# Performance work log

Measured on AMD Instinct MI355X. Metric: run time of the kernel, lower is better.

## Reference

```python
import jax, jax.numpy as jnp
import numpy as np

# Static architecture constants (match init_kwargs)
N, M, DIM = 2048, 4096, 256
KS = (0.9, 0.8, 0.7)
HEADS, BOT_HEADS = 4, 2
NEG_SLOPE = 0.2  # PyG GATConv default leaky-relu slope


def _p(key, shape, scale):
    return (scale * jax.random.normal(key, shape, dtype=jnp.float32))


def setup_inputs() -> dict:
    key = jax.random.key(0)
    ks = jax.random.split(key, 16)
    # Symmetric positive connectivity matrix (fMRI-like), fully dense
    R = jax.random.uniform(ks[0], (N, N), dtype=jnp.float32)
    A = 0.5 * (R + R.T)
    X = jax.random.normal(ks[1], (N, DIM), dtype=jnp.float32)
    s = 1.0 / np.sqrt(DIM).astype(np.float32)
    C, Cb = DIM // HEADS, DIM // BOT_HEADS
    inp = {
        'A': A, 'X': X,
        'W_down': _p(ks[2], (3, DIM, DIM), s),
        'as_down': _p(ks[3], (3, HEADS, C), s),
        'ad_down': _p(ks[4], (3, HEADS, C), s),
        'b_down': jnp.zeros((3, DIM), jnp.float32),
        'W_up': _p(ks[5], (3, DIM, DIM), s),
        'as_up': _p(ks[6], (3, HEADS, C), s),
        'ad_up': _p(ks[7], (3, HEADS, C), s),
        'b_up': jnp.zeros((3, DIM), jnp.float32),
        'W_bot': _p(ks[8], (DIM, DIM), s),
        'as_bot': _p(ks[9], (BOT_HEADS, Cb), s),
        'ad_bot': _p(ks[10], (BOT_HEADS, Cb), s),
        'b_bot': jnp.zeros((DIM,), jnp.float32),
        'W_pool': _p(ks[11], (3, DIM), s),
        'b_pool': jnp.zeros((3,), jnp.float32),
        'W_ups': _p(ks[12], (M, N), 1.0 / np.sqrt(N).astype(np.float32)),
        'b_ups': jnp.zeros((M,), jnp.float32),
    }
    return inp


def _sym_norm(A):
    # A_tilde = A + I ; D^{-1/2} A_tilde D^{-1/2} as elementwise broadcast
    A = A + jnp.eye(A.shape[0], dtype=A.dtype)
    d = A.sum(axis=1) + 1e-5
    di = d ** -0.5
    return di[:, None] * A * di[None, :]


def _gat(A, X, W, a_src, a_dst, b):
    # Dense-masked GATConv (concat=True, eval mode => no dropout).
    # Edge j->i exists iff A[j, i] > 0 (dense_to_sparse row=src, col=tgt).
    n = X.shape[0]
    H, C = a_src.shape
    x = (X @ W).reshape(n, H, C)                       # [n, H, C]
    s = jnp.einsum('nhc,hc->nh', x, a_src)             # source logit term
    t = jnp.einsum('nhc,hc->nh', x, a_dst)             # target logit term
    logits = jax.nn.leaky_relu(t[:, None, :] + s[None, :, :], NEG_SLOPE)  # [i, j, h]
    mask = (A.T > 0)[:, :, None]
    attn = jax.nn.softmax(jnp.where(mask, logits, -jnp.inf), axis=1)
    out = jnp.einsum('ijh,jhc->ihc', attn, x).reshape(n, H * C) + b
    return jax.nn.relu(out)


def reference(A, X, W_down, as_down, ad_down, b_down,
              W_up, as_up, ad_up, b_up,
              W_bot, as_bot, ad_bot, b_bot,
              W_pool, b_pool, W_ups, b_ups):
    A = _sym_norm(A)
    A_hist, idx_hist = [], []
    # Encoder: GAT -> top-k pool (gather rows/cols)
    for i in range(3):
        X = _gat(A, X, W_down[i], as_down[i], ad_down[i], b_down[i])
        A_hist.append(A)
        scores = jax.nn.sigmoid(X @ W_pool[i] + b_pool[i])
        k = max(2, int(KS[i] * A.shape[0]))            # static sizes
        vals, idx = jax.lax.top_k(scores, k)
        X = X[idx] * vals[:, None]
        A = A[idx][:, idx]
        idx_hist.append(idx)
    X = _gat(A, X, W_bot, as_bot, ad_bot, b_bot)
    # Decoder: scatter-unpool -> GAT -> adjacency reconstruction
    for i in range(3):
        u = 2 - i
        A, idx = A_hist[u], idx_hist[u]
        Xn = jnp.zeros((A.shape[0], X.shape[1]), X.dtype).at[idx].set(X)
        X = _gat(A, Xn, W_up[i], as_up[i], ad_up[i], b_up[i])
    # Upsampler: Linear(n->m) on X^T, then A_up = relu(Xu Xu^T)
    X_up = W_ups @ X + b_ups[:, None]                  # [M, DIM]
    A_up = jax.nn.relu(X_up @ X_up.T)                  # [M, M]
    return A_up
```

## Files before the change

### kernel.cpp

```cpp
#include <hip/hip_runtime.h>
#include <math.h>

#define NEG 0.2f
#define NMAX 2048
#define CHUNK 64
#define NCHMAX 32

__device__ __forceinline__ float lrelu(float v) { return v > 0.f ? v : NEG * v; }
__device__ __forceinline__ unsigned fenc(float v) {
    unsigned u = __float_as_uint(v);
    return (u & 0x80000000u) ? ~u : (u | 0x80000000u);
}
__device__ __forceinline__ float fdec(unsigned u) {
    return (u & 0x80000000u) ? __uint_as_float(u ^ 0x80000000u) : __uint_as_float(~u);
}

__global__ __launch_bounds__(256) void gemm_ks(const float* __restrict__ A,
                                               const float* __restrict__ B,
                                               float* __restrict__ C,
                                               const int* __restrict__ rowmapA,
                                               const float* __restrict__ rowscale,
                                               const int* __restrict__ rowmapC,
                                               int M, int N, int K) {
    __shared__ float As[16][68];
    __shared__ float Bs[16][68];
    const int tid = threadIdx.x;
    const int m0 = blockIdx.x * 64, n0 = blockIdx.y * 64;
    const int kchunk = K / gridDim.z;
    const int kbeg = blockIdx.z * kchunk, kend = kbeg + kchunk;
    const int tm = tid >> 4, tn = tid & 15;
    const int lr = tid >> 2, lc4 = (tid & 3) * 4;
    const int br = tid >> 4, bc4 = (tid & 15) * 4;
    const int am = m0 + lr;
    const bool aval = am < M;
    int arow = 0; float ascale = 1.f;
    if (aval) { arow = rowmapA ? rowmapA[am] : am; if (rowscale) ascale = rowscale[arow]; }
    const float* Ap = A + (size_t)arow * K;
    float4 va = make_float4(0.f, 0.f, 0.f, 0.f), vb;
    if (aval) va = *(const float4*)(Ap + kbeg + lc4);
    vb = *(const float4*)(B + (size_t)(kbeg + br) * N + n0 + bc4);
    float acc[4][4] = {{0.f}};
    for (int k0 = kbeg; k0 < kend; k0 += 16) {
        As[lc4 + 0][lr] = va.x * ascale; As[lc4 + 1][lr] = va.y * ascale;
        As[lc4 + 2][lr] = va.z * ascale; As[lc4 + 3][lr] = va.w * ascale;
        *(float4*)&Bs[br][bc4] = vb;
        __syncthreads();
        if (k0 + 16 < kend) {
            if (aval) va = *(const float4*)(Ap + k0 + 16 + lc4);
            vb = *(const float4*)(B + (size_t)(k0 + 16 + br) * N + n0 + bc4);
        }
#pragma unroll
        for (int kk = 0; kk < 16; ++kk) {
            float a[4], b[4];
            *(float4*)a = *(const float4*)&As[kk][tm * 4];
            *(float4*)b = *(const float4*)&Bs[kk][tn * 4];
#pragma unroll
            for (int x = 0; x < 4; ++x)
#pragma unroll
                for (int y = 0; y < 4; ++y) acc[x][y] = fmaf(a[x], b[y], acc[x][y]);
        }
        __syncthreads();
    }
#pragma unroll
    for (int x = 0; x < 4; ++x) {
        int m = m0 + tm * 4 + x;
        if (m >= M) continue;
        int orow = rowmapC ? rowmapC[m] : m;
        float* dst = C + (size_t)orow * N + n0 + tn * 4;
#pragma unroll
        for (int y = 0; y < 4; ++y) atomicAdd(dst + y, acc[x][y]);
    }
}

__global__ __launch_bounds__(256) void st_kernel(const float* __restrict__ xw,
                                                 const float* __restrict__ asrc,
                                                 const float* __restrict__ adst,
                                                 float* __restrict__ S, float* __restrict__ T,
                                                 unsigned* __restrict__ SMX,
                                                 int n, int Hh, int Cc) {
    int gid = blockIdx.x * 256 + threadIdx.x;
    int i = gid / Hh, h = gid - i * Hh;
    float s = -INFINITY;
    if (i < n) {
        const float* xr = xw + (size_t)i * 256 + h * Cc;
        const float* pa = asrc + h * Cc;
        const float* pd = adst + h * Cc;
        float sv = 0.f, tv = 0.f;
        for (int c = 0; c < Cc; c += 4) {
            float4 xv = *(const float4*)(xr + c);
            float4 av = *(const float4*)(pa + c);
            float4 dv = *(const float4*)(pd + c);
            sv += xv.x * av.x + xv.y * av.y + xv.z * av.z + xv.w * av.w;
            tv += xv.x * dv.x + xv.y * dv.y + xv.z * dv.z + xv.w * dv.w;
        }
        S[(size_t)i * Hh + h] = sv;
        T[(size_t)i * Hh + h] = tv;
        s = sv;
    }
    for (int off = Hh; off < 64; off <<= 1) s = fmaxf(s, __shfl_xor(s, off));
    int lane = threadIdx.x & 63;
    if (lane < Hh && s > -INFINITY) atomicMax(SMX + lane, fenc(s));
}

__global__ __launch_bounds__(256) void rank_k(const float* __restrict__ S,
                                              float* __restrict__ SS, int* __restrict__ PERM,
                                              int n, int Hh) {
    __shared__ float s[NMAX];
    int h = blockIdx.y;
    for (int j = threadIdx.x; j < n; j += 256) s[j] = S[(size_t)j * Hh + h];
    __syncthreads();
    int i = blockIdx.x * 256 + threadIdx.x;
    if (i >= n) return;
    float v = s[i];
    int cnt = 0, j = 0;
    for (; j + 4 <= n; j += 4) {
        float4 sv = *(const float4*)&s[j];
        cnt += (sv.x > v) || (sv.x == v && (j + 0) < i);
        cnt += (sv.y > v) || (sv.y == v && (j + 1) < i);
        cnt += (sv.z > v) || (sv.z == v && (j + 2) < i);
        cnt += (sv.w > v) || (sv.w == v && (j + 3) < i);
    }
    for (; j < n; ++j) {
        float sj = s[j];
        cnt += (sj > v) || (sj == v && j < i);
    }
    SS[h * NMAX + cnt] = v;
    PERM[h * NMAX + cnt] = i;
}

__global__ __launch_bounds__(256) void chunk_k(const float* __restrict__ XW,
                                               const float* __restrict__ SS,
                                               const int* __restrict__ PERM,
                                               const unsigned* __restrict__ SMX,
                                               float* __restrict__ TOT1, float* __restrict__ TOT2,
                                               float* __restrict__ ZT1, float* __restrict__ ZT2,
                                               int n, int Cc) {
    const int h = blockIdx.x, ch = blockIdx.y;
    const int nh = 256 / Cc, seg = CHUNK / nh;
    const int c = threadIdx.x % Cc, half = threadIdx.x / Cc;
    __shared__ float ssh[CHUNK];
    __shared__ int pjh[CHUNK];
    __shared__ float red1[256], red2[256];
    __shared__ float zr1[4], zr2[4];
    if (threadIdx.x < CHUNK) {
        int rk = ch * CHUNK + threadIdx.x;
        ssh[threadIdx.x] = (rk < n) ? SS[h * NMAX + rk] : 0.f;
        pjh[threadIdx.x] = (rk < n) ? PERM[h * NMAX + rk] : -1;
    }
    __syncthreads();
    const float smax = fdec(SMX[h]);
    float t1 = 0.f, t2 = 0.f, z1 = 0.f, z2 = 0.f;
#pragma unroll 4
    for (int q = 0; q < seg; ++q) {
        int r = half * seg + q;
        int j = pjh[r];
        if (j < 0) continue;
        float d = ssh[r] - smax;
        float w1 = expf(d), w2 = expf(NEG * d);
        float x = XW[(size_t)j * 256 + h * Cc + c];
        t1 = fmaf(w1, x, t1); t2 = fmaf(w2, x, t2);
        z1 += w1; z2 += w2;
    }
    red1[threadIdx.x] = t1; red2[threadIdx.x] = t2;
    if (c == 0) { zr1[half] = z1; zr2[half] = z2; }
    __syncthreads();
    if (half == 0) {
        for (int hh = 1; hh < nh; ++hh) { t1 += red1[hh * Cc + c]; t2 += red2[hh * Cc + c]; }
        TOT1[((size_t)h * NCHMAX + ch) * Cc + c] = t1;
        TOT2[((size_t)h * NCHMAX + ch) * Cc + c] = t2;
        if (c == 0) {
            float a = z1, b = z2;
            for (int hh = 1; hh < nh; ++hh) { a += zr1[hh]; b += zr2[hh]; }
            ZT1[h * NCHMAX + ch] = a;
            ZT2[h * NCHMAX + ch] = b;
        }
    }
}

__global__ __launch_bounds__(256) void combine_k(
    const float* __restrict__ XW, const float* __restrict__ SS,
    const int* __restrict__ PERM, const unsigned* __restrict__ SMX,
    const float* __restrict__ T,
    const float* __restrict__ TOT1, const float* __restrict__ TOT2,
    const float* __restrict__ ZT1, const float* __restrict__ ZT2,
    const float* __restrict__ bias, const float* __restrict__ Wp,
    const float* __restrict__ bp,
    float* __restrict__ Xout, float* __restrict__ SC, int n, int Hh, int nch) {
    const int i = blockIdx.x, t = threadIdx.x;
    const int C = 256 / Hh;
    __shared__ float f1s[4], f2s[4], invs[4], smaxs[4];
    __shared__ int qs[4], chs[4];
    __shared__ float coef[256];
    __shared__ int permsh[256];
    __shared__ float redw[4];
    float z1p = 0.f, z2s = 0.f;
    if (t < Hh) {
        int h = t;
        float smax = fdec(SMX[h]);
        smaxs[h] = smax;
        float tv = T[(size_t)i * Hh + h];
        float u = tv + smax, m = lrelu(u);
        f1s[h] = expf(u - m);
        f2s[h] = expf(NEG * u - m);
        float thr = -tv;
        int lo = 0, hi = n;
        while (lo < hi) {
            int mid = (lo + hi) >> 1;
            if (SS[h * NMAX + mid] > thr) lo = mid + 1; else hi = mid;
        }
        int q = lo;
        int ch = min(q / CHUNK, nch - 1);
        qs[h] = q; chs[h] = ch;
        for (int cc = 0; cc < ch; ++cc) z1p += ZT1[h * NCHMAX + cc];
        for (int cc = ch + 1; cc < nch; ++cc) z2s += ZT2[h * NCHMAX + cc];
    }
    __syncthreads();
    if (t < Hh * CHUNK) {
        int h = t >> 6, r = t & 63;
        int rank = chs[h] * CHUNK + r;
        float w = 0.f; int j = 0;
        if (rank < n) {
            float ssv = SS[h * NMAX + rank];
            j = PERM[h * NMAX + rank];
            float d = ssv - smaxs[h];
            w = (rank < qs[h]) ? f1s[h] * expf(d) : f2s[h] * expf(NEG * d);
        }
        coef[t] = w; permsh[t] = j;
    }
    __syncthreads();
    if (t < Hh) {
        int h = t;
        float den = fmaf(f1s[h], z1p, f2s[h] * z2s);
        for (int r = 0; r < CHUNK; ++r) den += coef[h * CHUNK + r];
        invs[h] = 1.f / den;
    }
    __syncthreads();
    const int h = t / C, c = t - h * C;
    const float* xcol = XW + h * C + c;
    float csum = 0.f;
#pragma unroll 8
    for (int r = 0; r < CHUNK; ++r)
        csum = fmaf(coef[h * CHUNK + r], xcol[(size_t)permsh[h * CHUNK + r] * 256], csum);
    float a1 = 0.f, a2 = 0.f;
    const int ch = chs[h];
    for (int cc = 0; cc < ch; ++cc) a1 += TOT1[((size_t)h * NCHMAX + cc) * C + c];
    for (int cc = ch + 1; cc < nch; ++cc) a2 += TOT2[((size_t)h * NCHMAX + cc) * C + c];
    float out = (fmaf(f1s[h], a1, f2s[h] * a2) + csum) * invs[h] + bias[t];
    out = fmaxf(out, 0.f);
    Xout[(size_t)i * 256 + t] = out;
    if (Wp) {
        float v = out * Wp[t];
#pragma unroll
        for (int off = 32; off; off >>= 1) v += __shfl_xor(v, off);
        if ((t & 63) == 0) redw[t >> 6] = v;
        __syncthreads();
        if (t == 0)
            SC[i] = 1.f / (1.f + expf(-(redw[0] + redw[1] + redw[2] + redw[3] + bp[0])));
    }
}

__global__ __launch_bounds__(256) void topk_k(const float* __restrict__ SC,
                                              int* __restrict__ IDX, int n, int k) {
    __shared__ float s[NMAX];
    for (int j = threadIdx.x; j < n; j += 256) s[j] = SC[j];
    __syncthreads();
    int i = blockIdx.x * 256 + threadIdx.x;
    if (i >= n) return;
    float v = s[i];
    int cnt = 0, j = 0;
    for (; j + 4 <= n; j += 4) {
        float4 sv = *(const float4*)&s[j];
        cnt += (sv.x > v) || (sv.x == v && (j + 0) < i);
        cnt += (sv.y > v) || (sv.y == v && (j + 1) < i);
        cnt += (sv.z > v) || (sv.z == v && (j + 2) < i);
        cnt += (sv.w > v) || (sv.w == v && (j + 3) < i);
    }
    for (; j < n; ++j) {
        float sj = s[j];
        cnt += (sj > v) || (sj == v && j < i);
    }
    if (cnt < k) IDX[cnt] = i;
}

__global__ __launch_bounds__(256) void ttr_sym(const float* __restrict__ A,
                                               const float* __restrict__ bias,
                                               float* __restrict__ C, int M, int K) {
    const int L = blockIdx.x;
    int by = (int)((sqrtf(8.f * L + 1.f) - 1.f) * 0.5f);
    while ((by + 1) * (by + 2) / 2 <= L) ++by;
    while (by * (by + 1) / 2 > L) --by;
    const int bx = L - by * (by + 1) / 2;
    __shared__ float As[16][132];
    __shared__ float Bs[16][132];
    const int tid = threadIdx.x;
    const int m0 = bx * 128, n0 = by * 128;
    const int lr = tid >> 1, lc8 = (tid & 1) * 8;
    const int tm = tid >> 4, tn = tid & 15;
    const float ab = bias[m0 + lr], bb = bias[n0 + lr];
    const float* Ar = A + (size_t)(m0 + lr) * K;
    const float* Br = A + (size_t)(n0 + lr) * K;
    float4 va0 = *(const float4*)(Ar + lc8), va1 = *(const float4*)(Ar + lc8 + 4);
    float4 vb0 = *(const float4*)(Br + lc8), vb1 = *(const float4*)(Br + lc8 + 4);
    float acc[8][8] = {{0.f}};
    for (int k0 = 0; k0 < K; k0 += 16) {
        As[lc8 + 0][lr] = va0.x + ab; As[lc8 + 1][lr] = va0.y + ab;
        As[lc8 + 2][lr] = va0.z + ab; As[lc8 + 3][lr] = va0.w + ab;
        As[lc8 + 4][lr] = va1.x + ab; As[lc8 + 5][lr] = va1.y + ab;
        As[lc8 + 6][lr] = va1.z + ab; As[lc8 + 7][lr] = va1.w + ab;
        Bs[lc8 + 0][lr] = vb0.x + bb; Bs[lc8 + 1][lr] = vb0.y + bb;
        Bs[lc8 + 2][lr] = vb0.z + bb; Bs[lc8 + 3][lr] = vb0.w + bb;
        Bs[lc8 + 4][lr] = vb1.x + bb; Bs[lc8 + 5][lr] = vb1.y + bb;
        Bs[lc8 + 6][lr] = vb1.z + bb; Bs[lc8 + 7][lr] = vb1.w + bb;
        __syncthreads();
        if (k0 + 16 < K) {
            va0 = *(const float4*)(Ar + k0 + 16 + lc8); va1 = *(const float4*)(Ar + k0 + 20 + lc8);
            vb0 = *(const float4*)(Br + k0 + 16 + lc8); vb1 = *(const float4*)(Br + k0 + 20 + lc8);
        }
#pragma unroll
        for (int kk = 0; kk < 16; ++kk) {
            float a[8], b[8];
            *(float4*)&a[0] = *(const float4*)&As[kk][tm * 4];
            *(float4*)&a[4] = *(const float4*)&As[kk][64 + tm * 4];
            *(float4*)&b[0] = *(const float4*)&Bs[kk][tn * 4];
            *(float4*)&b[4] = *(const float4*)&Bs[kk][64 + tn * 4];
#pragma unroll
            for (int x = 0; x < 8; ++x)
#pragma unroll
                for (int y = 0; y < 8; ++y) acc[x][y] = fmaf(a[x], b[y], acc[x][y]);
        }
        __syncthreads();
    }
#pragma unroll
    for (int x = 0; x < 8; ++x)
#pragma unroll
        for (int y = 0; y < 8; ++y) acc[x][y] = fmaxf(acc[x][y], 0.f);
#pragma unroll
    for (int x = 0; x < 8; ++x) {
        int row = m0 + ((x < 4) ? tm * 4 + x : 64 + tm * 4 + (x - 4));
        float* dst = C + (size_t)row * M + n0;
        *(float4*)(dst + tn * 4) = make_float4(acc[x][0], acc[x][1], acc[x][2], acc[x][3]);
        *(float4*)(dst + 64 + tn * 4) = make_float4(acc[x][4], acc[x][5], acc[x][6], acc[x][7]);
    }
    if (bx != by) {
#pragma unroll
        for (int y = 0; y < 8; ++y) {
            int row = n0 + ((y < 4) ? tn * 4 + y : 64 + tn * 4 + (y - 4));
            float* dst = C + (size_t)row * M + m0;
            *(float4*)(dst + tm * 4) = make_float4(acc[0][y], acc[1][y], acc[2][y], acc[3][y]);
            *(float4*)(dst + 64 + tm * 4) = make_float4(acc[4][y], acc[5][y], acc[6][y], acc[7][y]);
        }
    }
}

extern "C" void kernel_launch(void* const* d_in, const int* in_sizes, int n_in,
                              void* d_out, int out_size, void* d_ws, size_t ws_size,
                              hipStream_t stream) {
    const float* X0      = (const float*)d_in[1];
    const float* W_down  = (const float*)d_in[2];
    const float* as_down = (const float*)d_in[3];
    const float* ad_down = (const float*)d_in[4];
    const float* b_down  = (const float*)d_in[5];
    const float* W_up    = (const float*)d_in[6];
    const float* as_up   = (const float*)d_in[7];
    const float* ad_up   = (const float*)d_in[8];
    const float* b_up    = (const float*)d_in[9];
    const float* W_bot   = (const float*)d_in[10];
    const float* as_bot  = (const float*)d_in[11];
    const float* ad_bot  = (const float*)d_in[12];
    const float* b_bot   = (const float*)d_in[13];
    const float* W_pool  = (const float*)d_in[14];
    const float* b_pool  = (const float*)d_in[15];
    const float* W_ups   = (const float*)d_in[16];
    const float* b_ups   = (const float*)d_in[17];
    float* out = (float*)d_out;

    float* F = (float*)d_ws;
    size_t o = 0;
    float* Xb  = F + o; o += 2048 * 256;
    float* XW  = F + o; o += 2048 * 256;
    unsigned* SMX = (unsigned*)(F + o); o += 16;
    float* S   = F + o; o += 2048 * 4;
    float* T   = F + o; o += 2048 * 4;
    float* SS  = F + o; o += 2048 * 4;
    int* PERM  = (int*)(F + o); o += 2048 * 4;
    float* TOT1 = F + o; o += 8192;
    float* TOT2 = F + o; o += 8192;
    float* ZT1 = F + o; o += 128;
    float* ZT2 = F + o; o += 128;
    float* SC  = F + o; o += 2048;
    int* IDXs[3];
    IDXs[0] = (int*)(F + o); o += 2048;
    IDXs[1] = (int*)(F + o); o += 2048;
    IDXs[2] = (int*)(F + o); o += 2048;
    float* XU  = F + o; o += 4096 * 256;

    auto cdiv = [](int a, int b) { return (a + b - 1) / b; };

    auto run_gat = [&](const float* Xin, int Mrows, int n, const float* W,
                       const float* asrc, const float* adst, const float* bias, int Hh,
                       const int* rmA, const float* rscale, const int* rmC,
                       const float* Wp, const float* bp) {
        int C = 256 / Hh;
        int nch = cdiv(n, CHUNK);
        hipMemsetAsync(XW, 0, (size_t)(2048 * 256 + 16) * 4, stream);
        gemm_ks<<<dim3(cdiv(Mrows, 64), 4, 4), 256, 0, stream>>>(Xin, W, XW, rmA, rscale,
                                                                 rmC, Mrows, 256, 256);
        st_kernel<<<cdiv(n * Hh, 256), 256, 0, stream>>>(XW, asrc, adst, S, T, SMX, n, Hh, C);
        rank_k<<<dim3(cdiv(n, 256), Hh), 256, 0, stream>>>(S, SS, PERM, n, Hh);
        chunk_k<<<dim3(Hh, nch), 256, 0, stream>>>(XW, SS, PERM, SMX, TOT1, TOT2, ZT1, ZT2,
                                                   n, C);
        combine_k<<<n, 256, 0, stream>>>(XW, SS, PERM, SMX, T, TOT1, TOT2, ZT1, ZT2, bias,
                                         Wp, bp, Xb, SC, n, Hh, nch);
    };

    const int ns[4] = {2048, 1843, 1474, 1031};

    for (int l = 0; l < 3; ++l) {
        int n = ns[l], k = ns[l + 1];
        run_gat(l ? Xb : X0, n, n, W_down + (size_t)l * 65536, as_down + l * 256,
                ad_down + l * 256, b_down + l * 256, 4,
                l ? IDXs[l - 1] : nullptr, l ? SC : nullptr, nullptr,
                W_pool + l * 256, b_pool + l);
        topk_k<<<cdiv(n, 256), 256, 0, stream>>>(SC, IDXs[l], n, k);
    }

    run_gat(Xb, ns[3], ns[3], W_bot, as_bot, ad_bot, b_bot, 2, IDXs[2], SC, nullptr,
            nullptr, nullptr);

    for (int i = 0; i < 3; ++i) {
        int u = 2 - i;
        int pn = ns[u], kc = ns[u + 1];
        run_gat(Xb, kc, pn, W_up + (size_t)i * 65536, as_up + i * 256, ad_up + i * 256,
                b_up + i * 256, 4, nullptr, nullptr, IDXs[u], nullptr, nullptr);
    }

    hipMemsetAsync(XU, 0, (size_t)4096 * 256 * 4, stream);
    gemm_ks<<<dim3(64, 4, 4), 256, 0, stream>>>(W_ups, Xb, XU, nullptr, nullptr, nullptr,
                                                4096, 256, 2048);
    ttr_sym<<<528, 256, 0, stream>>>(XU, b_ups, out, 4096, 256);
}
```

Before: 1.183 ms.

## Fuse GAT projection with attention logits and drop split-K atomics and memsets

```diff
diff --git a/kernel.cpp b/kernel.cpp
--- a/kernel.cpp
+++ b/kernel.cpp
@@ -7,47 +7,45 @@
 #define NCHMAX 32
 
 __device__ __forceinline__ float lrelu(float v) { return v > 0.f ? v : NEG * v; }
-__device__ __forceinline__ unsigned fenc(float v) {
-    unsigned u = __float_as_uint(v);
-    return (u & 0x80000000u) ? ~u : (u | 0x80000000u);
-}
-__device__ __forceinline__ float fdec(unsigned u) {
-    return (u & 0x80000000u) ? __uint_as_float(u ^ 0x80000000u) : __uint_as_float(~u);
-}
-
-__global__ __launch_bounds__(256) void gemm_ks(const float* __restrict__ A,
+
+template <bool DOST>
+__global__ __launch_bounds__(256) void gemm_st(const float* __restrict__ A,
                                                const float* __restrict__ B,
                                                float* __restrict__ C,
                                                const int* __restrict__ rowmapA,
                                                const float* __restrict__ rowscale,
-                                               const int* __restrict__ rowmapC,
-                                               int M, int N, int K) {
+                                               const float* __restrict__ asrc,
+                                               const float* __restrict__ adst,
+                                               float* __restrict__ S, float* __restrict__ T,
+                                               int M, int K, int Hh) {
     __shared__ float As[16][68];
     __shared__ float Bs[16][68];
+    __shared__ float Sred[64][17];
+    __shared__ float Tred[64][17];
     const int tid = threadIdx.x;
     const int m0 = blockIdx.x * 64, n0 = blockIdx.y * 64;
-    const int kchunk = K / gridDim.z;
-    const int kbeg = blockIdx.z * kchunk, kend = kbeg + kchunk;
     const int tm = tid >> 4, tn = tid & 15;
     const int lr = tid >> 2, lc4 = (tid & 3) * 4;
     const int br = tid >> 4, bc4 = (tid & 15) * 4;
     const int am = m0 + lr;
-    const bool aval = am < M;
-    int arow = 0; float ascale = 1.f;
-    if (aval) { arow = rowmapA ? rowmapA[am] : am; if (rowscale) ascale = rowscale[arow]; }
+    bool aval = am < M;
+    int arow = am;
+    float ascale = 1.f;
+    if (aval && rowmapA) { arow = rowmapA[am]; if (arow < 0) { aval = false; arow = 0; } }
+    if (aval && rowscale) ascale = rowscale[arow];
     const float* Ap = A + (size_t)arow * K;
-    float4 va = make_float4(0.f, 0.f, 0.f, 0.f), vb;
-    if (aval) va = *(const float4*)(Ap + kbeg + lc4);
-    vb = *(const float4*)(B + (size_t)(kbeg + br) * N + n0 + bc4);
+    float4 va = make_float4(0.f, 0.f, 0.f, 0.f);
+    if (aval) va = *(const float4*)(Ap + lc4);
+    float4 vb = *(const float4*)(B + (size_t)br * 256 + n0 + bc4);
     float acc[4][4] = {{0.f}};
-    for (int k0 = kbeg; k0 < kend; k0 += 16) {
+    for (int k0 = 0; k0 < K; k0 += 16) {
         As[lc4 + 0][lr] = va.x * ascale; As[lc4 + 1][lr] = va.y * ascale;
         As[lc4 + 2][lr] = va.z * ascale; As[lc4 + 3][lr] = va.w * ascale;
         *(float4*)&Bs[br][bc4] = vb;
         __syncthreads();
-        if (k0 + 16 < kend) {
+        if (k0 + 16 < K) {
             if (aval) va = *(const float4*)(Ap + k0 + 16 + lc4);
-            vb = *(const float4*)(B + (size_t)(k0 + 16 + br) * N + n0 + bc4);
+            vb = *(const float4*)(B + (size_t)(k0 + 16 + br) * 256 + n0 + bc4);
         }
 #pragma unroll
         for (int kk = 0; kk < 16; ++kk) {
@@ -64,11 +62,32 @@
 #pragma unroll
     for (int x = 0; x < 4; ++x) {
         int m = m0 + tm * 4 + x;
-        if (m >= M) continue;
-        int orow = rowmapC ? rowmapC[m] : m;
-        float* dst = C + (size_t)orow * N + n0 + tn * 4;
-#pragma unroll
-        for (int y = 0; y < 4; ++y) atomicAdd(dst + y, acc[x][y]);
+        if (m < M)
+            *(float4*)(C + (size_t)m * 256 + n0 + tn * 4) =
+                make_float4(acc[x][0], acc[x][1], acc[x][2], acc[x][3]);
+    }
+    if (DOST) {
+        const int h = blockIdx.y;
+        float4 a4 = *(const float4*)(asrc + h * 64 + tn * 4);
+        float4 d4 = *(const float4*)(adst + h * 64 + tn * 4);
+#pragma unroll
+        for (int x = 0; x < 4; ++x) {
+            Sred[tm * 4 + x][tn] = acc[x][0] * a4.x + acc[x][1] * a4.y +
+                                   acc[x][2] * a4.z + acc[x][3] * a4.w;
+            Tred[tm * 4 + x][tn] = acc[x][0] * d4.x + acc[x][1] * d4.y +
+                                   acc[x][2] * d4.z + acc[x][3] * d4.w;
+        }
+        __syncthreads();
+        if (tid < 64) {
+            int m = m0 + tid;
+            if (m < M) {
+                float s = 0.f, t = 0.f;
+#pragma unroll
+                for (int q = 0; q < 16; ++q) { s += Sred[tid][q]; t += Tred[tid][q]; }
+                S[(size_t)m * Hh + h] = s;
+                T[(size_t)m * Hh + h] = t;
+            }
+        }
     }
 }
 
@@ -76,30 +95,23 @@
                                                  const float* __restrict__ asrc,
                                                  const float* __restrict__ adst,
                                                  float* __restrict__ S, float* __restrict__ T,
-                                                 unsigned* __restrict__ SMX,
                                                  int n, int Hh, int Cc) {
     int gid = blockIdx.x * 256 + threadIdx.x;
     int i = gid / Hh, h = gid - i * Hh;
-    float s = -INFINITY;
-    if (i < n) {
-        const float* xr = xw + (size_t)i * 256 + h * Cc;
-        const float* pa = asrc + h * Cc;
-        const float* pd = adst + h * Cc;
-        float sv = 0.f, tv = 0.f;
-        for (int c = 0; c < Cc; c += 4) {
-            float4 xv = *(const float4*)(xr + c);
-            float4 av = *(const float4*)(pa + c);
-            float4 dv = *(const float4*)(pd + c);
-            sv += xv.x * av.x + xv.y * av.y + xv.z * av.z + xv.w * av.w;
-            tv += xv.x * dv.x + xv.y * dv.y + xv.z * dv.z + xv.w * dv.w;
-        }
-        S[(size_t)i * Hh + h] = sv;
-        T[(size_t)i * Hh + h] = tv;
-        s = sv;
-    }
-    for (int off = Hh; off < 64; off <<= 1) s = fmaxf(s, __shfl_xor(s, off));
-    int lane = threadIdx.x & 63;
-    if (lane < Hh && s > -INFINITY) atomicMax(SMX + lane, fenc(s));
+    if (i >= n) return;
+    const float* xr = xw + (size_t)i * 256 + h * Cc;
+    const float* pa = asrc + h * Cc;
+    const float* pd = adst + h * Cc;
+    float sv = 0.f, tv = 0.f;
+    for (int c = 0; c < Cc; c += 4) {
+        float4 xv = *(const float4*)(xr + c);
+        float4 av = *(const float4*)(pa + c);
+        float4 dv = *(const float4*)(pd + c);
+        sv += xv.x * av.x + xv.y * av.y + xv.z * av.z + xv.w * av.w;
+        tv += xv.x * dv.x + xv.y * dv.y + xv.z * dv.z + xv.w * dv.w;
+    }
+    S[(size_t)i * Hh + h] = sv;
+    T[(size_t)i * Hh + h] = tv;
 }
 
 __global__ __launch_bounds__(256) void rank_k(const float* __restrict__ S,
@@ -131,7 +143,6 @@
 __global__ __launch_bounds__(256) void chunk_k(const float* __restrict__ XW,
                                                const float* __restrict__ SS,
                                                const int* __restrict__ PERM,
-                                               const unsigned* __restrict__ SMX,
                                                float* __restrict__ TOT1, float* __restrict__ TOT2,
                                                float* __restrict__ ZT1, float* __restrict__ ZT2,
                                                int n, int Cc) {
@@ -148,7 +159,7 @@
         pjh[threadIdx.x] = (rk < n) ? PERM[h * NMAX + rk] : -1;
     }
     __syncthreads();
-    const float smax = fdec(SMX[h]);
+    const float smax = SS[h * NMAX];
     float t1 = 0.f, t2 = 0.f, z1 = 0.f, z2 = 0.f;
 #pragma unroll 4
     for (int q = 0; q < seg; ++q) {
@@ -179,8 +190,7 @@
 
 __global__ __launch_bounds__(256) void combine_k(
     const float* __restrict__ XW, const float* __restrict__ SS,
-    const int* __restrict__ PERM, const unsigned* __restrict__ SMX,
-    const float* __restrict__ T,
+    const int* __restrict__ PERM, const float* __restrict__ T,
     const float* __restrict__ TOT1, const float* __restrict__ TOT2,
     const float* __restrict__ ZT1, const float* __restrict__ ZT2,
     const float* __restrict__ bias, const float* __restrict__ Wp,
@@ -196,7 +206,7 @@
     float z1p = 0.f, z2s = 0.f;
     if (t < Hh) {
         int h = t;
-        float smax = fdec(SMX[h]);
+        float smax = SS[h * NMAX];
         smaxs[h] = smax;
         float tv = T[(size_t)i * Hh + h];
         float u = tv + smax, m = lrelu(u);
@@ -260,7 +270,8 @@
 }
 
 __global__ __launch_bounds__(256) void topk_k(const float* __restrict__ SC,
-                                              int* __restrict__ IDX, int n, int k) {
+                                              int* __restrict__ IDX, int* __restrict__ INV,
+                                              int n, int k) {
     __shared__ float s[NMAX];
     for (int j = threadIdx.x; j < n; j += 256) s[j] = SC[j];
     __syncthreads();
@@ -279,7 +290,66 @@
         float sj = s[j];
         cnt += (sj > v) || (sj == v && j < i);
     }
-    if (cnt < k) IDX[cnt] = i;
+    if (cnt < k) { IDX[cnt] = i; INV[i] = cnt; }
+    else INV[i] = -1;
+}
+
+__global__ __launch_bounds__(256) void gemm128a(const float* __restrict__ A,
+                                                const float* __restrict__ B,
+                                                float* __restrict__ C,
+                                                int M, int N, int K) {
+    __shared__ float As[16][132];
+    __shared__ float Bs[16][132];
+    const int tid = threadIdx.x;
+    const int m0 = blockIdx.x * 128, n0 = blockIdx.y * 128;
+    const int kchunk = K / gridDim.z;
+    const int kbeg = blockIdx.z * kchunk, kend = kbeg + kchunk;
+    const int lr = tid >> 1, lc8 = (tid & 1) * 8;
+    const int br = tid >> 4, bn8 = (tid & 15) * 8;
+    const int tm = tid >> 4, tn = tid & 15;
+    const float* Ar = A + (size_t)(m0 + lr) * K;
+    float4 va0 = *(const float4*)(Ar + kbeg + lc8), va1 = *(const float4*)(Ar + kbeg + lc8 + 4);
+    float4 vb0 = *(const float4*)(B + (size_t)(kbeg + br) * N + n0 + bn8);
+    float4 vb1 = *(const float4*)(B + (size_t)(kbeg + br) * N + n0 + bn8 + 4);
+    float acc[8][8] = {{0.f}};
+    for (int k0 = kbeg; k0 < kend; k0 += 16) {
+        As[lc8 + 0][lr] = va0.x; As[lc8 + 1][lr] = va0.y;
+        As[lc8 + 2][lr] = va0.z; As[lc8 + 3][lr] = va0.w;
+        As[lc8 + 4][lr] = va1.x; As[lc8 + 5][lr] = va1.y;
+        As[lc8 + 6][lr] = va1.z; As[lc8 + 7][lr] = va1.w;
+        *(float4*)&Bs[br][bn8] = vb0;
+        *(float4*)&Bs[br][bn8 + 4] = vb1;
+        __syncthreads();
+        if (k0 + 16 < kend) {
+            va0 = *(const float4*)(Ar + k0 + 16 + lc8);
+            va1 = *(const float4*)(Ar + k0 + 20 + lc8);
+            vb0 = *(const float4*)(B + (size_t)(k0 + 16 + br) * N + n0 + bn8);
+            vb1 = *(const float4*)(B + (size_t)(k0 + 16 + br) * N + n0 + bn8 + 4);
+        }
+#pragma unroll
+        for (int kk = 0; kk < 16; ++kk) {
+            float a[8], b[8];
+            *(float4*)&a[0] = *(const float4*)&As[kk][tm * 4];
+            *(float4*)&a[4] = *(const float4*)&As[kk][64 + tm * 4];
+            *(float4*)&b[0] = *(const float4*)&Bs[kk][tn * 4];
+            *(float4*)&b[4] = *(const float4*)&Bs[kk][64 + tn * 4];
+#pragma unroll
+            for (int x = 0; x < 8; ++x)
+#pragma unroll
+                for (int y = 0; y < 8; ++y) acc[x][y] = fmaf(a[x], b[y], acc[x][y]);
+        }
+        __syncthreads();
+    }
+#pragma unroll
+    for (int x = 0; x < 8; ++x) {
+        int row = m0 + ((x < 4) ? tm * 4 + x : 64 + tm * 4 + (x - 4));
+        float* dst = C + (size_t)row * N + n0;
+#pragma unroll
+        for (int y = 0; y < 8; ++y) {
+            int col = (y < 4) ? tn * 4 + y : 64 + tn * 4 + (y - 4);
+            atomicAdd(dst + col, acc[x][y]);
+        }
+    }
 }
 
 __global__ __launch_bounds__(256) void ttr_sym(const float* __restrict__ A,
@@ -378,7 +448,6 @@
     size_t o = 0;
     float* Xb  = F + o; o += 2048 * 256;
     float* XW  = F + o; o += 2048 * 256;
-    unsigned* SMX = (unsigned*)(F + o); o += 16;
     float* S   = F + o; o += 2048 * 4;
     float* T   = F + o; o += 2048 * 4;
     float* SS  = F + o; o += 2048 * 4;
@@ -388,28 +457,35 @@
     float* ZT1 = F + o; o += 128;
     float* ZT2 = F + o; o += 128;
     float* SC  = F + o; o += 2048;
-    int* IDXs[3];
+    int* IDXs[3]; int* INVs[3];
     IDXs[0] = (int*)(F + o); o += 2048;
     IDXs[1] = (int*)(F + o); o += 2048;
     IDXs[2] = (int*)(F + o); o += 2048;
+    INVs[0] = (int*)(F + o); o += 2048;
+    INVs[1] = (int*)(F + o); o += 2048;
+    INVs[2] = (int*)(F + o); o += 2048;
     float* XU  = F + o; o += 4096 * 256;
 
     auto cdiv = [](int a, int b) { return (a + b - 1) / b; };
 
-    auto run_gat = [&](const float* Xin, int Mrows, int n, const float* W,
+    auto run_gat = [&](const float* Xin, int n, const float* W,
                        const float* asrc, const float* adst, const float* bias, int Hh,
-                       const int* rmA, const float* rscale, const int* rmC,
+                       const int* rmA, const float* rscale,
                        const float* Wp, const float* bp) {
         int C = 256 / Hh;
         int nch = cdiv(n, CHUNK);
-        hipMemsetAsync(XW, 0, (size_t)(2048 * 256 + 16) * 4, stream);
-        gemm_ks<<<dim3(cdiv(Mrows, 64), 4, 4), 256, 0, stream>>>(Xin, W, XW, rmA, rscale,
-                                                                 rmC, Mrows, 256, 256);
-        st_kernel<<<cdiv(n * Hh, 256), 256, 0, stream>>>(XW, asrc, adst, S, T, SMX, n, Hh, C);
+        if (Hh == 4) {
+            hipLaunchKernelGGL((gemm_st<true>), dim3(cdiv(n, 64), 4), dim3(256), 0, stream,
+                               Xin, W, XW, rmA, rscale, asrc, adst, S, T, n, 256, Hh);
+        } else {
+            hipLaunchKernelGGL((gemm_st<false>), dim3(cdiv(n, 64), 4), dim3(256), 0, stream,
+                               Xin, W, XW, rmA, rscale, nullptr, nullptr, nullptr, nullptr,
+                               n, 256, Hh);
+            st_kernel<<<cdiv(n * Hh, 256), 256, 0, stream>>>(XW, asrc, adst, S, T, n, Hh, C);
+        }
         rank_k<<<dim3(cdiv(n, 256), Hh), 256, 0, stream>>>(S, SS, PERM, n, Hh);
-        chunk_k<<<dim3(Hh, nch), 256, 0, stream>>>(XW, SS, PERM, SMX, TOT1, TOT2, ZT1, ZT2,
-                                                   n, C);
-        combine_k<<<n, 256, 0, stream>>>(XW, SS, PERM, SMX, T, TOT1, TOT2, ZT1, ZT2, bias,
+        chunk_k<<<dim3(Hh, nch), 256, 0, stream>>>(XW, SS, PERM, TOT1, TOT2, ZT1, ZT2, n, C);
+        combine_k<<<n, 256, 0, stream>>>(XW, SS, PERM, T, TOT1, TOT2, ZT1, ZT2, bias,
                                          Wp, bp, Xb, SC, n, Hh, nch);
     };
 
@@ -417,25 +493,23 @@
 
     for (int l = 0; l < 3; ++l) {
         int n = ns[l], k = ns[l + 1];
-        run_gat(l ? Xb : X0, n, n, W_down + (size_t)l * 65536, as_down + l * 256,
+        run_gat(l ? Xb : X0, n, W_down + (size_t)l * 65536, as_down + l * 256,
                 ad_down + l * 256, b_down + l * 256, 4,
-                l ? IDXs[l - 1] : nullptr, l ? SC : nullptr, nullptr,
+                l ? IDXs[l - 1] : nullptr, l ? SC : nullptr,
                 W_pool + l * 256, b_pool + l);
-        topk_k<<<cdiv(n, 256), 256, 0, stream>>>(SC, IDXs[l], n, k);
-    }
-
-    run_gat(Xb, ns[3], ns[3], W_bot, as_bot, ad_bot, b_bot, 2, IDXs[2], SC, nullptr,
-            nullptr, nullptr);
+        topk_k<<<cdiv(n, 256), 256, 0, stream>>>(SC, IDXs[l], INVs[l], n, k);
+    }
+
+    run_gat(Xb, ns[3], W_bot, as_bot, ad_bot, b_bot, 2, IDXs[2], SC, nullptr, nullptr);
 
     for (int i = 0; i < 3; ++i) {
         int u = 2 - i;
-        int pn = ns[u], kc = ns[u + 1];
-        run_gat(Xb, kc, pn, W_up + (size_t)i * 65536, as_up + i * 256, ad_up + i * 256,
-                b_up + i * 256, 4, nullptr, nullptr, IDXs[u], nullptr, nullptr);
+        int pn = ns[u];
+        run_gat(Xb, pn, W_up + (size_t)i * 65536, as_up + i * 256, ad_up + i * 256,
+                b_up + i * 256, 4, INVs[u], nullptr, nullptr, nullptr);
     }
 
     hipMemsetAsync(XU, 0, (size_t)4096 * 256 * 4, stream);
-    gemm_ks<<<dim3(64, 4, 4), 256, 0, stream>>>(W_ups, Xb, XU, nullptr, nullptr, nullptr,
-                                                4096, 256, 2048);
+    gemm128a<<<dim3(32, 2, 8), 256, 0, stream>>>(W_ups, Xb, XU, 4096, 256, 2048);
     ttr_sym<<<528, 256, 0, stream>>>(XU, b_ups, out, 4096, 256);
 }
```

Measured after the change: 1.093 ms. 1.08x faster.
